# Kernel optimization log

Hardware: AMD Instinct MI355X
Metric: run time of the kernel (lower is better)

## Reference

```python
import jax, jax.numpy as jnp
import numpy as np

N_TOKEN = 392
POS_WEIGHT = 1.0
LOSS_WEIGHT = 1.0


def _cam_map(logits, w_proj, xf, shape):
    # logits: (B, K_cls); w_proj: (K_cls, C); xf: (B, C, N)
    B, T, H, W = shape
    top_cls = jnp.argmax(logits, axis=1)                 # sort desc -> [0] == argmax
    w_top = w_proj[top_cls]                              # (B, C) gather top-class weight row
    row = jnp.einsum('bc,bcn->bn', w_top, xf)            # (B, N) per-sample CAM scores
    mn = row.min(axis=1, keepdims=True)
    mx = row.max(axis=1, keepdims=True)
    rown = (row - mn) / (mx - mn)                        # min-max normalize
    vals, idxs = jax.lax.top_k(rown, N_TOKEN)            # (B, 392)
    hw = H * W
    ti = idxs // hw
    hi = (idxs % hw) // W
    wi = idxs % W
    bi = jnp.broadcast_to(jnp.arange(B)[:, None], idxs.shape)
    cam = jnp.zeros((B, T, H, W), rown.dtype).at[bi, ti, hi, wi].set(vals)
    return cam


def _forward(x, pred_v_logits, pred_n_logits, w_proj_v, w_proj_n,
             conv_w, conv_b, score_w, score_b):
    B, C, T, H, W = x.shape
    xf = x.reshape(B, C, T * H * W)
    cam_v = _cam_map(pred_v_logits, w_proj_v, xf, (B, T, H, W))
    cam_n = _cam_map(pred_n_logits, w_proj_n, xf, (B, T, H, W))
    cam_gt = jnp.maximum(cam_v, cam_n)                   # torch.where(v > n, v, n)
    cam_gt = jax.lax.stop_gradient(cam_gt)               # original builds it from numpy + .detach()

    dn = ('NCDHW', 'OIDHW', 'NCDHW')
    h1 = jax.nn.relu(
        jax.lax.conv_general_dilated(x, conv_w, (1, 1, 1),
                                     [(0, 0), (1, 1), (1, 1)],
                                     dimension_numbers=dn)
        + conv_b[None, :, None, None, None])
    logits = (jax.lax.conv_general_dilated(h1, score_w, (1, 1, 1),
                                           [(0, 0), (0, 0), (0, 0)],
                                           dimension_numbers=dn)
              + score_b[None, :, None, None, None])      # (B,1,T,H,W)

    xcam = logits[:, 0].reshape(B * T, H * W)
    y = cam_gt.reshape(B * T, H * W)
    # BCEWithLogitsLoss(pos_weight) mean
    bce = -(POS_WEIGHT * y * jax.nn.log_sigmoid(xcam)
            + (1.0 - y) * jax.nn.log_sigmoid(-xcam))
    return LOSS_WEIGHT * bce.mean()


def setup_inputs() -> dict:
    key = jax.random.key(0)
    ks = jax.random.split(key, 8)
    B, C, T, H, W = 64, 256, 32, 7, 7
    Kv, Kn, D = 97, 300, 512
    x = jax.random.normal(ks[0], (B, C, T, H, W), jnp.float32)
    pred_v_logits = jax.random.normal(ks[1], (B, Kv), jnp.float32)
    pred_n_logits = jax.random.normal(ks[2], (B, Kn), jnp.float32)
    w_proj_v = jax.random.normal(ks[3], (Kv, C), jnp.float32) / np.sqrt(C)
    w_proj_n = jax.random.normal(ks[4], (Kn, C), jnp.float32) / np.sqrt(C)
    conv_w = jax.random.normal(ks[5], (D, C, 1, 3, 3), jnp.float32) / np.sqrt(C * 9)
    conv_b = jnp.zeros((D,), jnp.float32)
    score_w = jax.random.normal(ks[6], (1, D, 1, 1, 1), jnp.float32) / np.sqrt(D)
    score_b = jnp.zeros((1,), jnp.float32)
    return {"x": x, "pred_v_logits": pred_v_logits, "pred_n_logits": pred_n_logits,
            "w_proj_v": w_proj_v, "w_proj_n": w_proj_n,
            "conv_w": conv_w, "conv_b": conv_b,
            "score_w": score_w, "score_b": score_b}


def reference(x, pred_v_logits, pred_n_logits, w_proj_v, w_proj_n,
              conv_w, conv_b, score_w, score_b):
    return _forward(x, pred_v_logits, pred_n_logits, w_proj_v, w_proj_n,
                    conv_w, conv_b, score_w, score_b)
```

## Files before the change

### kernel.cpp

```cpp
#include <hip/hip_runtime.h>
#include <hip/hip_bf16.h>
#include <math.h>

#define BB 64
#define CC 256
#define TT 32
#define HH 7
#define WW 7
#define HW 49
#define NN 1568
#define KV 97
#define KN 300
#define DD 512
#define NTOK 392
#define TOTAL (BB*TT*HW)
#define BCAP 256

typedef float f32x4 __attribute__((ext_vector_type(4)));
typedef short bf16x8 __attribute__((ext_vector_type(8)));

#define GLDS(g, l) __builtin_amdgcn_global_load_lds(                          \
    (const __attribute__((address_space(1))) void*)(g),                       \
    (__attribute__((address_space(3))) void*)(l), 16, 0, 0)

__global__ __launch_bounds__(256, 3) void k_tr(
        const float* __restrict__ x, __hip_bfloat16* __restrict__ xp,
        const float* __restrict__ cw, __hip_bfloat16* __restrict__ wb,
        int* __restrict__ counter) {
    __shared__ unsigned short xs[98 * 256];
    int bid = blockIdx.x;
    int tid = threadIdx.x;
    if (bid == 0 && tid == 0) *counter = 0;

    {
        int base = bid * 1152;
        #pragma unroll
        for (int r = 0; r < 5; ++r) {
            int o = base + r * 256 + tid;
            if (o < base + 1152) {
                int kk = o / (DD * CC);
                int rem = o - kk * (DD * CC);
                int d = rem >> 8, c = rem & 255;
                wb[o] = __float2bfloat16(cw[(d * CC + c) * 9 + kk]);
            }
        }
    }

    int b  = bid >> 4;
    int tp = bid & 15;
    int t0 = tp << 1;

    const float2* src = (const float2*)(x + ((size_t)(b * CC + tid) * TT + t0) * HW);
    #pragma unroll 1
    for (int r = 0; r < 6; ++r) {
        float2 v[8];
        #pragma unroll
        for (int j = 0; j < 8; ++j) v[j] = src[r * 8 + j];
        #pragma unroll
        for (int j = 0; j < 8; ++j) {
            int q = (r * 8 + j) * 2;
            __hip_bfloat16 b0 = __float2bfloat16(v[j].x);
            __hip_bfloat16 b1 = __float2bfloat16(v[j].y);
            xs[q * 256 + tid] = *reinterpret_cast<unsigned short*>(&b0);
            xs[(q + 1) * 256 + tid] = *reinterpret_cast<unsigned short*>(&b1);
        }
    }
    {
        float2 v = src[48];
        __hip_bfloat16 b0 = __float2bfloat16(v.x);
        __hip_bfloat16 b1 = __float2bfloat16(v.y);
        xs[96 * 256 + tid] = *reinterpret_cast<unsigned short*>(&b0);
        xs[97 * 256 + tid] = *reinterpret_cast<unsigned short*>(&b1);
    }
    __syncthreads();

    __hip_bfloat16* xpb = xp + (size_t)(b * TT + t0) * 81 * 256;
    const bf16x8 zero = (bf16x8){0, 0, 0, 0, 0, 0, 0, 0};
    for (int u = tid; u < 5184; u += 256) {
        int pos = u >> 5, c0 = (u & 31) * 8;
        int f = pos / 81, p = pos - f * 81;
        int hh = p / 9, ww = p - (p / 9) * 9;
        bf16x8 val = zero;
        if (hh >= 1 && hh <= 7 && ww >= 1 && ww <= 7) {
            int q = f * 49 + (hh - 1) * 7 + (ww - 1);
            val = *reinterpret_cast<const bf16x8*>(xs + q * 256 + c0);
        }
        *reinterpret_cast<bf16x8*>(xpb + (size_t)u * 8) = val;
    }
}

__device__ __forceinline__ int binof(float v) {
    int i = (int)(v * 1024.f);
    return i < 0 ? 0 : (i > 1023 ? 1023 : i);
}

__device__ void cam_block(int b, int tid, char* smem,
                          const float* __restrict__ x,
                          const float* __restrict__ pv, const float* __restrict__ pn,
                          const float* __restrict__ wpv, const float* __restrict__ wpn,
                          float* __restrict__ cam) {
    float* rv = (float*)smem;
    float* rn = (float*)(smem + 6272);
    int* h = (int*)(smem + 12544);
    int* tsum = (int*)(smem + 16640);
    float* lval_v = (float*)(smem + 17664);
    int* lidx_v = (int*)(smem + 18688);
    float* lval_n = (float*)(smem + 19712);
    int* lidx_n = (int*)(smem + 20736);
    float* wred = (float*)(smem + 21760);
    int* sc = (int*)(smem + 21824);
    float* wvs = (float*)(smem + 21888);
    float* wns = (float*)(smem + 22912);
    int* cls2 = (int*)(smem + 23936);

    int lane = tid & 63;
    if (tid < 128) {
        int head = tid >> 6;
        const float* r = head ? (pn + b * KN) : (pv + b * KV);
        int K = head ? KN : KV;
        float best = -1e30f; int bi = 0x7fffffff;
        for (int k = lane; k < K; k += 64) {
            float v = r[k];
            if (v > best || (v == best && k < bi)) { best = v; bi = k; }
        }
        #pragma unroll
        for (int off = 32; off >= 1; off >>= 1) {
            float ov = __shfl_xor(best, off);
            int oi = __shfl_xor(bi, off);
            if (ov > best || (ov == best && oi < bi)) { best = ov; bi = oi; }
        }
        if (lane == 0) cls2[head] = bi;
    }
    __syncthreads();
    wvs[tid] = wpv[cls2[0] * CC + tid];
    wns[tid] = wpn[cls2[1] * CC + tid];
    __syncthreads();

    {
        const f32x4* xb4 = (const f32x4*)(x + (size_t)b * CC * NN);
        bool two = tid < (392 - 256);
        f32x4 av0 = {0.f,0.f,0.f,0.f}, an0 = {0.f,0.f,0.f,0.f};
        f32x4 av1 = {0.f,0.f,0.f,0.f}, an1 = {0.f,0.f,0.f,0.f};
        for (int c = 0; c < CC; ++c) {
            float wv = wvs[c], wn = wns[c];
            const f32x4* rowc = xb4 + (size_t)c * 392;
            f32x4 u0 = rowc[tid];
            #pragma unroll
            for (int r = 0; r < 4; ++r) {
                av0[r] = fmaf(wv, u0[r], av0[r]);
                an0[r] = fmaf(wn, u0[r], an0[r]);
            }
            if (two) {
                f32x4 u1 = rowc[tid + 256];
                #pragma unroll
                for (int r = 0; r < 4; ++r) {
                    av1[r] = fmaf(wv, u1[r], av1[r]);
                    an1[r] = fmaf(wn, u1[r], an1[r]);
                }
            }
        }
        *reinterpret_cast<f32x4*>(rv + 4 * tid) = av0;
        *reinterpret_cast<f32x4*>(rn + 4 * tid) = an0;
        if (two) {
            *reinterpret_cast<f32x4*>(rv + 4 * (tid + 256)) = av1;
            *reinterpret_cast<f32x4*>(rn + 4 * (tid + 256)) = an1;
        }
    }
    __syncthreads();

    float mnv = 1e30f, mxv = -1e30f, mnn = 1e30f, mxn = -1e30f;
    for (int n = tid; n < NN; n += 256) {
        float v = rv[n]; mnv = fminf(mnv, v); mxv = fmaxf(mxv, v);
        float u = rn[n]; mnn = fminf(mnn, u); mxn = fmaxf(mxn, u);
    }
    #pragma unroll
    for (int off = 32; off >= 1; off >>= 1) {
        mnv = fminf(mnv, __shfl_xor(mnv, off));
        mxv = fmaxf(mxv, __shfl_xor(mxv, off));
        mnn = fminf(mnn, __shfl_xor(mnn, off));
        mxn = fmaxf(mxn, __shfl_xor(mxn, off));
    }
    if ((tid & 63) == 0) {
        int wid = tid >> 6;
        wred[wid * 4 + 0] = mnv; wred[wid * 4 + 1] = mxv;
        wred[wid * 4 + 2] = mnn; wred[wid * 4 + 3] = mxn;
    }
    if (tid == 0) { sc[0] = 0; sc[1] = 0; }
    __syncthreads();
    mnv = fminf(fminf(wred[0], wred[4]), fminf(wred[8], wred[12]));
    mxv = fmaxf(fmaxf(wred[1], wred[5]), fmaxf(wred[9], wred[13]));
    mnn = fminf(fminf(wred[2], wred[6]), fminf(wred[10], wred[14]));
    mxn = fmaxf(fmaxf(wred[3], wred[7]), fmaxf(wred[11], wred[15]));
    float iv = 1.f / (mxv - mnv), inn = 1.f / (mxn - mnn);

    for (int n = tid; n < NN; n += 256) {
        rv[n] = (rv[n] - mnv) * iv;
        rn[n] = (rn[n] - mnn) * inn;
    }
    for (int i = tid; i < 1024; i += 256) h[i] = 0;
    __syncthreads();
    for (int n = tid; n < NN; n += 256) {
        atomicAdd(&h[binof(rv[n])], 1);
        atomicAdd(&h[binof(rn[n])], 1 << 16);
    }
    __syncthreads();

    int h0 = h[4 * tid], h1 = h[4 * tid + 1], h2 = h[4 * tid + 2], h3 = h[4 * tid + 3];
    tsum[tid] = h0 + h1 + h2 + h3;
    __syncthreads();
    for (int off = 1; off < 256; off <<= 1) {
        int add = (tid + off < 256) ? tsum[tid + off] : 0;
        __syncthreads();
        tsum[tid] += add;
        __syncthreads();
    }
    {
        int scur = tsum[tid];
        int hk[4] = {h0, h1, h2, h3};
        #pragma unroll
        for (int k = 0; k < 4; ++k) {
            int snext = scur - hk[k];
            int scv = scur & 0xffff, ncv = snext & 0xffff;
            int sh = scur >> 16, nh = snext >> 16;
            if (scv >= NTOK && ncv < NTOK) { sc[2] = 4 * tid + k; sc[3] = ncv; }
            if (sh >= NTOK && nh < NTOK) { sc[4] = 4 * tid + k; sc[5] = nh; }
            scur = snext;
        }
    }
    __syncthreads();
    int bsv = sc[2], abv = sc[3], bsn = sc[4], abn = sc[5];

    for (int n = tid; n < NN; n += 256) {
        float v = rv[n]; int bv = binof(v);
        if (bv < bsv) rv[n] = 0.f;
        else if (bv == bsv) {
            int s = atomicAdd(&sc[0], 1);
            if (s < BCAP) { lval_v[s] = v; lidx_v[s] = n; }
        }
        float u = rn[n]; int bu = binof(u);
        if (bu < bsn) rn[n] = 0.f;
        else if (bu == bsn) {
            int s = atomicAdd(&sc[1], 1);
            if (s < BCAP) { lval_n[s] = u; lidx_n[s] = n; }
        }
    }
    __syncthreads();
    int Lv = sc[0] < BCAP ? sc[0] : BCAP;
    int Ln = sc[1] < BCAP ? sc[1] : BCAP;
    for (int i = tid; i < Lv; i += 256) {
        float vi = lval_v[i]; int ni = lidx_v[i]; int r = 0;
        for (int j = 0; j < Lv; ++j) {
            float vj = lval_v[j]; int nj = lidx_v[j];
            r += (vj > vi || (vj == vi && nj < ni)) ? 1 : 0;
        }
        rv[ni] = (r < NTOK - abv) ? vi : 0.f;
    }
    for (int i = tid; i < Ln; i += 256) {
        float vi = lval_n[i]; int ni = lidx_n[i]; int r = 0;
        for (int j = 0; j < Ln; ++j) {
            float vj = lval_n[j]; int nj = lidx_n[j];
            r += (vj > vi || (vj == vi && nj < ni)) ? 1 : 0;
        }
        rn[ni] = (r < NTOK - abn) ? vi : 0.f;
    }
    __syncthreads();
    for (int n = tid; n < NN; n += 256) cam[b * NN + n] = fmaxf(rv[n], rn[n]);
}

__global__ __launch_bounds__(256, 3) void k_gemm(
        const __hip_bfloat16* __restrict__ xp, const __hip_bfloat16* __restrict__ wb,
        const float* __restrict__ convb, const float* __restrict__ scorew,
        float* __restrict__ pl,
        const float* __restrict__ x,
        const float* __restrict__ pv, const float* __restrict__ pn,
        const float* __restrict__ wpv, const float* __restrict__ wpn,
        float* __restrict__ cam) {
    __shared__ char smem[32768];
    int tid = threadIdx.x;
    int bid = blockIdx.x;
    if (bid < 64) { cam_block(bid, tid, smem, x, pv, pn, wpv, wpn, cam); return; }
    char* As = smem;
    char* Bs = smem + 16384;
    int gid = bid - 64;
    int xcd = gid & 7;
    int local = gid >> 3;
    int mtile = xcd * 98 + (local >> 2);
    int nblk = local & 3;
    int m0 = mtile * 128;
    int n0 = nblk * 128;
    int lane = tid & 63, wv = tid >> 6;
    int wm = wv >> 1, wn = wv & 1;
    int ln = lane & 15, qd = lane >> 4;

    int rrow = tid >> 3;
    int segst = ((tid & 7) ^ (rrow & 7)) * 8;
    int bt_[4], hh_[4], ww_[4];
    const __hip_bfloat16* bptr[4];
    #pragma unroll
    for (int j = 0; j < 4; ++j) {
        int m = m0 + j * 32 + rrow;
        int bt = m / HW, q = m - bt * HW;
        bt_[j] = bt; hh_[j] = q / WW; ww_[j] = q - (q / WW) * WW;
        bptr[j] = wb + (size_t)(n0 + j * 32 + rrow) * 256 + segst;
    }

    int swz = ln & 7;
    int offk[2] = {((0 + qd) ^ swz) * 16, ((4 + qd) ^ swz) * 16};

    f32x4 acc[4][4];
    #pragma unroll
    for (int i = 0; i < 4; ++i)
        #pragma unroll
        for (int j = 0; j < 4; ++j) acc[i][j] = (f32x4){0.f, 0.f, 0.f, 0.f};

    for (int kk = 0; kk < 9; ++kk) {
        int kh = kk / 3, kw = kk - (kk / 3) * 3;
        const __hip_bfloat16* aptr[4];
        #pragma unroll
        for (int j = 0; j < 4; ++j)
            aptr[j] = xp + ((size_t)bt_[j] * 81 + (hh_[j] + kh) * 9 + (ww_[j] + kw)) * 256 + segst;
        const size_t boff = (size_t)kk * (DD * 256);
        #pragma unroll
        for (int c0 = 0; c0 < 256; c0 += 64) {
            __syncthreads();
            #pragma unroll
            for (int j = 0; j < 4; ++j) {
                GLDS(aptr[j] + c0, As + j * 4096 + tid * 16);
                GLDS(bptr[j] + boff + c0, Bs + j * 4096 + tid * 16);
            }
            __syncthreads();
            #pragma unroll
            for (int k2 = 0; k2 < 2; ++k2) {
                bf16x8 af[4], bfr[4];
                #pragma unroll
                for (int i = 0; i < 4; ++i)
                    af[i] = *(const bf16x8*)(As + (wm * 64 + i * 16 + ln) * 128 + offk[k2]);
                #pragma unroll
                for (int j = 0; j < 4; ++j)
                    bfr[j] = *(const bf16x8*)(Bs + (wn * 64 + j * 16 + ln) * 128 + offk[k2]);
                #pragma unroll
                for (int i = 0; i < 4; ++i)
                    #pragma unroll
                    for (int j = 0; j < 4; ++j)
                        acc[i][j] = __builtin_amdgcn_mfma_f32_16x16x32_bf16(af[i], bfr[j], acc[i][j], 0, 0, 0);
            }
        }
    }

    float swr[4], cbr[4];
    #pragma unroll
    for (int j = 0; j < 4; ++j) {
        int n = n0 + wn * 64 + j * 16 + ln;
        swr[j] = scorew[n];
        cbr[j] = convb[n];
    }
    float* dst = pl + (size_t)(nblk * 2 + wn) * TOTAL;
    #pragma unroll
    for (int i = 0; i < 4; ++i) {
        #pragma unroll
        for (int r = 0; r < 4; ++r) {
            float v = 0.f;
            #pragma unroll
            for (int j = 0; j < 4; ++j) {
                float h1 = acc[i][j][r] + cbr[j];
                h1 = h1 > 0.f ? h1 : 0.f;
                v = fmaf(swr[j], h1, v);
            }
            v += __shfl_xor(v, 1);
            v += __shfl_xor(v, 2);
            v += __shfl_xor(v, 4);
            v += __shfl_xor(v, 8);
            if (ln == 0)
                dst[m0 + wm * 64 + i * 16 + qd * 4 + r] = v;
        }
    }
}

__global__ __launch_bounds__(256) void k_bce(
        const float* __restrict__ pl, const float* __restrict__ cam,
        const float* __restrict__ sb, float* __restrict__ part,
        int* __restrict__ counter, float* __restrict__ out) {
    __shared__ float sbuf[256];
    __shared__ int isLast;
    int tid = threadIdx.x;
    int m = blockIdx.x * 256 + tid;
    float l = sb[0];
    #pragma unroll
    for (int s = 0; s < 8; ++s) l += pl[(size_t)s * TOTAL + m];
    float y = cam[m];
    float v = fmaxf(l, 0.f) - l * y + log1pf(expf(-fabsf(l)));
    sbuf[tid] = v; __syncthreads();
    for (int k = 128; k > 0; k >>= 1) {
        if (tid < k) sbuf[tid] += sbuf[tid + k];
        __syncthreads();
    }
    if (tid == 0) {
        part[blockIdx.x] = sbuf[0];
        __threadfence();
        int d = atomicAdd(counter, 1);
        isLast = (d == 391);
    }
    __syncthreads();
    if (isLast) {
        float s = 0.f;
        for (int i = tid; i < 392; i += 256) s += part[i];
        sbuf[tid] = s; __syncthreads();
        for (int k = 128; k > 0; k >>= 1) {
            if (tid < k) sbuf[tid] += sbuf[tid + k];
            __syncthreads();
        }
        if (tid == 0) out[0] = sbuf[0] * (1.0f / (float)TOTAL);
    }
}

extern "C" void kernel_launch(void* const* d_in, const int* in_sizes, int n_in,
                              void* d_out, int out_size, void* d_ws, size_t ws_size,
                              hipStream_t stream) {
    const float* x   = (const float*)d_in[0];
    const float* pv  = (const float*)d_in[1];
    const float* pn  = (const float*)d_in[2];
    const float* wpv = (const float*)d_in[3];
    const float* wpn = (const float*)d_in[4];
    const float* cw  = (const float*)d_in[5];
    const float* cb  = (const float*)d_in[6];
    const float* sw  = (const float*)d_in[7];
    const float* sb  = (const float*)d_in[8];

    char* w8 = (char*)d_ws;
    __hip_bfloat16* xp  = (__hip_bfloat16*)w8;
    __hip_bfloat16* wb  = (__hip_bfloat16*)(w8 + 84934656);
    float* pl      = (float*)(w8 + 87293952);
    float* cam     = (float*)(w8 + 90505216);
    float* part    = (float*)(w8 + 90906624);
    int*   counter = (int*)(w8 + 90908192);

    k_tr<<<1024, 256, 0, stream>>>(x, xp, cw, wb, counter);
    k_gemm<<<64 + 3136, 256, 0, stream>>>(xp, wb, cb, sw, pl,
                                          x, pv, pn, wpv, wpn, cam);
    k_bce<<<392, 256, 0, stream>>>(pl, cam, sb, part, counter, (float*)d_out);
}
```

Before: 432.7 us.

## Move CAM into transpose kernel and rebuild conv GEMM as 8-wave triple-buffered pipeline

The CAM blocks move out of the GEMM launch and into the transpose/pad kernel, so the GEMM grid is uniform. The conv GEMM becomes a 512-thread, 256x128-tile kernel with a three-slot LDS ring filled by direct global-to-LDS loads issued two stages ahead. Each stage is split into four MFMA phases that interleave fragment reads and next-stage loads, using barriers, waitcnt, sched_barrier and setprio to overlap memory with compute. The costs are much larger shared memory per block (lower occupancy), more barriers, and the epilogue must now handle the new tile mapping correctly.

```diff
diff --git a/kernel.cpp b/kernel.cpp
--- a/kernel.cpp
+++ b/kernel.cpp
@@ -23,71 +23,7 @@
     (const __attribute__((address_space(1))) void*)(g),                       \
     (__attribute__((address_space(3))) void*)(l), 16, 0, 0)
 
-__global__ __launch_bounds__(256, 3) void k_tr(
-        const float* __restrict__ x, __hip_bfloat16* __restrict__ xp,
-        const float* __restrict__ cw, __hip_bfloat16* __restrict__ wb,
-        int* __restrict__ counter) {
-    __shared__ unsigned short xs[98 * 256];
-    int bid = blockIdx.x;
-    int tid = threadIdx.x;
-    if (bid == 0 && tid == 0) *counter = 0;
-
-    {
-        int base = bid * 1152;
-        #pragma unroll
-        for (int r = 0; r < 5; ++r) {
-            int o = base + r * 256 + tid;
-            if (o < base + 1152) {
-                int kk = o / (DD * CC);
-                int rem = o - kk * (DD * CC);
-                int d = rem >> 8, c = rem & 255;
-                wb[o] = __float2bfloat16(cw[(d * CC + c) * 9 + kk]);
-            }
-        }
-    }
-
-    int b  = bid >> 4;
-    int tp = bid & 15;
-    int t0 = tp << 1;
-
-    const float2* src = (const float2*)(x + ((size_t)(b * CC + tid) * TT + t0) * HW);
-    #pragma unroll 1
-    for (int r = 0; r < 6; ++r) {
-        float2 v[8];
-        #pragma unroll
-        for (int j = 0; j < 8; ++j) v[j] = src[r * 8 + j];
-        #pragma unroll
-        for (int j = 0; j < 8; ++j) {
-            int q = (r * 8 + j) * 2;
-            __hip_bfloat16 b0 = __float2bfloat16(v[j].x);
-            __hip_bfloat16 b1 = __float2bfloat16(v[j].y);
-            xs[q * 256 + tid] = *reinterpret_cast<unsigned short*>(&b0);
-            xs[(q + 1) * 256 + tid] = *reinterpret_cast<unsigned short*>(&b1);
-        }
-    }
-    {
-        float2 v = src[48];
-        __hip_bfloat16 b0 = __float2bfloat16(v.x);
-        __hip_bfloat16 b1 = __float2bfloat16(v.y);
-        xs[96 * 256 + tid] = *reinterpret_cast<unsigned short*>(&b0);
-        xs[97 * 256 + tid] = *reinterpret_cast<unsigned short*>(&b1);
-    }
-    __syncthreads();
-
-    __hip_bfloat16* xpb = xp + (size_t)(b * TT + t0) * 81 * 256;
-    const bf16x8 zero = (bf16x8){0, 0, 0, 0, 0, 0, 0, 0};
-    for (int u = tid; u < 5184; u += 256) {
-        int pos = u >> 5, c0 = (u & 31) * 8;
-        int f = pos / 81, p = pos - f * 81;
-        int hh = p / 9, ww = p - (p / 9) * 9;
-        bf16x8 val = zero;
-        if (hh >= 1 && hh <= 7 && ww >= 1 && ww <= 7) {
-            int q = f * 49 + (hh - 1) * 7 + (ww - 1);
-            val = *reinterpret_cast<const bf16x8*>(xs + q * 256 + c0);
-        }
-        *reinterpret_cast<bf16x8*>(xpb + (size_t)u * 8) = val;
-    }
-}
+#define MFMA16(a, b, c) __builtin_amdgcn_mfma_f32_16x16x32_bf16(a, b, c, 0, 0, 0)
 
 __device__ __forceinline__ int binof(float v) {
     int i = (int)(v * 1024.f);
@@ -267,84 +203,227 @@
     for (int n = tid; n < NN; n += 256) cam[b * NN + n] = fmaxf(rv[n], rn[n]);
 }
 
-__global__ __launch_bounds__(256, 3) void k_gemm(
+__global__ __launch_bounds__(256, 3) void k_trcam(
+        const float* __restrict__ x, __hip_bfloat16* __restrict__ xp,
+        const float* __restrict__ cw, __hip_bfloat16* __restrict__ wb,
+        const float* __restrict__ pv, const float* __restrict__ pn,
+        const float* __restrict__ wpv, const float* __restrict__ wpn,
+        float* __restrict__ cam, int* __restrict__ counter) {
+    __shared__ char smem[50176];
+    int bid0 = blockIdx.x;
+    int tid = threadIdx.x;
+    if (bid0 < 64) { cam_block(bid0, tid, smem, x, pv, pn, wpv, wpn, cam); return; }
+    int bid = bid0 - 64;
+    unsigned short* xs = (unsigned short*)smem;
+    if (bid == 0 && tid == 0) *counter = 0;
+
+    {
+        int base = bid * 1152;
+        #pragma unroll
+        for (int r = 0; r < 5; ++r) {
+            int o = base + r * 256 + tid;
+            if (o < base + 1152) {
+                int kk = o / (DD * CC);
+                int rem = o - kk * (DD * CC);
+                int d = rem >> 8, c = rem & 255;
+                wb[o] = __float2bfloat16(cw[(d * CC + c) * 9 + kk]);
+            }
+        }
+    }
+
+    int b  = bid >> 4;
+    int tp = bid & 15;
+    int t0 = tp << 1;
+
+    const float2* src = (const float2*)(x + ((size_t)(b * CC + tid) * TT + t0) * HW);
+    #pragma unroll 1
+    for (int r = 0; r < 6; ++r) {
+        float2 v[8];
+        #pragma unroll
+        for (int j = 0; j < 8; ++j) v[j] = src[r * 8 + j];
+        #pragma unroll
+        for (int j = 0; j < 8; ++j) {
+            int q = (r * 8 + j) * 2;
+            __hip_bfloat16 b0 = __float2bfloat16(v[j].x);
+            __hip_bfloat16 b1 = __float2bfloat16(v[j].y);
+            xs[q * 256 + tid] = *reinterpret_cast<unsigned short*>(&b0);
+            xs[(q + 1) * 256 + tid] = *reinterpret_cast<unsigned short*>(&b1);
+        }
+    }
+    {
+        float2 v = src[48];
+        __hip_bfloat16 b0 = __float2bfloat16(v.x);
+        __hip_bfloat16 b1 = __float2bfloat16(v.y);
+        xs[96 * 256 + tid] = *reinterpret_cast<unsigned short*>(&b0);
+        xs[97 * 256 + tid] = *reinterpret_cast<unsigned short*>(&b1);
+    }
+    __syncthreads();
+
+    __hip_bfloat16* xpb = xp + (size_t)(b * TT + t0) * 81 * 256;
+    const bf16x8 zero = (bf16x8){0, 0, 0, 0, 0, 0, 0, 0};
+    for (int u = tid; u < 5184; u += 256) {
+        int pos = u >> 5, c0 = (u & 31) * 8;
+        int f = pos / 81, p = pos - f * 81;
+        int hh = p / 9, ww = p - (p / 9) * 9;
+        bf16x8 val = zero;
+        if (hh >= 1 && hh <= 7 && ww >= 1 && ww <= 7) {
+            int q = f * 49 + (hh - 1) * 7 + (ww - 1);
+            val = *reinterpret_cast<const bf16x8*>(xs + q * 256 + c0);
+        }
+        *reinterpret_cast<bf16x8*>(xpb + (size_t)u * 8) = val;
+    }
+}
+
+__global__ __launch_bounds__(512, 2) void k_gemm8(
         const __hip_bfloat16* __restrict__ xp, const __hip_bfloat16* __restrict__ wb,
         const float* __restrict__ convb, const float* __restrict__ scorew,
-        float* __restrict__ pl,
-        const float* __restrict__ x,
-        const float* __restrict__ pv, const float* __restrict__ pn,
-        const float* __restrict__ wpv, const float* __restrict__ wpn,
-        float* __restrict__ cam) {
-    __shared__ char smem[32768];
+        float* __restrict__ pl) {
+    __shared__ char smem[147456];
     int tid = threadIdx.x;
     int bid = blockIdx.x;
-    if (bid < 64) { cam_block(bid, tid, smem, x, pv, pn, wpv, wpn, cam); return; }
-    char* As = smem;
-    char* Bs = smem + 16384;
-    int gid = bid - 64;
-    int xcd = gid & 7;
-    int local = gid >> 3;
-    int mtile = xcd * 98 + (local >> 2);
+    int xcd = bid & 7;
+    int local = bid >> 3;
+    int mtile = xcd * 49 + (local >> 2);
     int nblk = local & 3;
-    int m0 = mtile * 128;
+    int m0 = mtile * 256;
     int n0 = nblk * 128;
     int lane = tid & 63, wv = tid >> 6;
     int wm = wv >> 1, wn = wv & 1;
     int ln = lane & 15, qd = lane >> 4;
-
-    int rrow = tid >> 3;
-    int segst = ((tid & 7) ^ (rrow & 7)) * 8;
-    int bt_[4], hh_[4], ww_[4];
-    const __hip_bfloat16* bptr[4];
-    #pragma unroll
-    for (int j = 0; j < 4; ++j) {
-        int m = m0 + j * 32 + rrow;
-        int bt = m / HW, q = m - bt * HW;
-        bt_[j] = bt; hh_[j] = q / WW; ww_[j] = q - (q / WW) * WW;
-        bptr[j] = wb + (size_t)(n0 + j * 32 + rrow) * 256 + segst;
-    }
-
     int swz = ln & 7;
+
+    int srow = tid >> 3, sseg = tid & 7;
+    int swseg = (sseg ^ (srow & 7)) * 8;
+    unsigned aoff[4];
+    #pragma unroll
+    for (int q = 0; q < 4; ++q) {
+        int m = m0 + q * 64 + srow;
+        int bt = m / HW, qq = m - bt * HW;
+        int hh = qq / WW, ww = qq - (qq / WW) * WW;
+        aoff[q] = (unsigned)(bt * 81 + (hh + 1) * 9 + (ww + 1) - 10) * 256 + swseg;
+    }
+    unsigned boff[2];
+    #pragma unroll
+    for (int q = 0; q < 2; ++q)
+        boff[q] = (unsigned)(n0 + q * 64 + srow) * 256 + swseg;
+
+    auto STAGE = [&](int s, int part) {
+        int kk = s >> 2;
+        int kh = kk / 3, kw = kk - kh * 3;
+        unsigned c0 = (unsigned)((s & 3) << 6);
+        int buf = s - (s / 3) * 3;
+        char* base = smem + buf * 49152;
+        if (part < 2) {
+            unsigned so = (unsigned)(kh * 9 + kw) * 256 + c0;
+            #pragma unroll
+            for (int u = 0; u < 2; ++u) {
+                int q = part * 2 + u;
+                GLDS(xp + (size_t)(aoff[q] + so), base + q * 8192 + tid * 16);
+            }
+        } else {
+            unsigned so = (unsigned)kk * (DD * 256) + c0;
+            #pragma unroll
+            for (int u = 0; u < 2; ++u)
+                GLDS(wb + (size_t)(boff[u] + so), base + 32768 + u * 8192 + tid * 16);
+        }
+    };
+
+    f32x4 acc[4][4];
+    #pragma unroll
+    for (int i = 0; i < 4; ++i)
+        #pragma unroll
+        for (int j = 0; j < 4; ++j) acc[i][j] = (f32x4){0.f, 0.f, 0.f, 0.f};
+
     int offk[2] = {((0 + qd) ^ swz) * 16, ((4 + qd) ^ swz) * 16};
 
-    f32x4 acc[4][4];
-    #pragma unroll
-    for (int i = 0; i < 4; ++i)
-        #pragma unroll
-        for (int j = 0; j < 4; ++j) acc[i][j] = (f32x4){0.f, 0.f, 0.f, 0.f};
-
-    for (int kk = 0; kk < 9; ++kk) {
-        int kh = kk / 3, kw = kk - (kk / 3) * 3;
-        const __hip_bfloat16* aptr[4];
-        #pragma unroll
-        for (int j = 0; j < 4; ++j)
-            aptr[j] = xp + ((size_t)bt_[j] * 81 + (hh_[j] + kh) * 9 + (ww_[j] + kw)) * 256 + segst;
-        const size_t boff = (size_t)kk * (DD * 256);
-        #pragma unroll
-        for (int c0 = 0; c0 < 256; c0 += 64) {
-            __syncthreads();
-            #pragma unroll
-            for (int j = 0; j < 4; ++j) {
-                GLDS(aptr[j] + c0, As + j * 4096 + tid * 16);
-                GLDS(bptr[j] + boff + c0, Bs + j * 4096 + tid * 16);
-            }
-            __syncthreads();
-            #pragma unroll
-            for (int k2 = 0; k2 < 2; ++k2) {
-                bf16x8 af[4], bfr[4];
+    STAGE(0, 0); STAGE(0, 1); STAGE(0, 2);
+    STAGE(1, 0); STAGE(1, 1); STAGE(1, 2);
+    asm volatile("s_waitcnt vmcnt(6)" ::: "memory");
+    __builtin_amdgcn_s_barrier();
+
+    #pragma unroll 1
+    for (int s = 0; s < 36; ++s) {
+        const char* Ab = smem + (s - (s / 3) * 3) * 49152;
+        const char* Bb = Ab + 32768;
+        bool more = s < 34;
+        bf16x8 af[2][2], b0r[2][2], b1r[2][2];
+
+        #pragma unroll
+        for (int i = 0; i < 2; ++i)
+            #pragma unroll
+            for (int k2 = 0; k2 < 2; ++k2)
+                af[i][k2] = *(const bf16x8*)(Ab + (wm * 64 + i * 16 + ln) * 128 + offk[k2]);
+        #pragma unroll
+        for (int j = 0; j < 2; ++j)
+            #pragma unroll
+            for (int k2 = 0; k2 < 2; ++k2)
+                b0r[j][k2] = *(const bf16x8*)(Bb + (wn * 64 + j * 16 + ln) * 128 + offk[k2]);
+        if (more) STAGE(s + 2, 0);
+        __builtin_amdgcn_s_barrier();
+        asm volatile("s_waitcnt lgkmcnt(0)" ::: "memory");
+        __builtin_amdgcn_sched_barrier(0);
+        __builtin_amdgcn_s_setprio(1);
+        #pragma unroll
+        for (int i = 0; i < 2; ++i)
+            #pragma unroll
+            for (int j = 0; j < 2; ++j)
                 #pragma unroll
-                for (int i = 0; i < 4; ++i)
-                    af[i] = *(const bf16x8*)(As + (wm * 64 + i * 16 + ln) * 128 + offk[k2]);
+                for (int k2 = 0; k2 < 2; ++k2)
+                    acc[i][j] = MFMA16(af[i][k2], b0r[j][k2], acc[i][j]);
+        __builtin_amdgcn_s_setprio(0);
+
+        #pragma unroll
+        for (int j = 0; j < 2; ++j)
+            #pragma unroll
+            for (int k2 = 0; k2 < 2; ++k2)
+                b1r[j][k2] = *(const bf16x8*)(Bb + (wn * 64 + (j + 2) * 16 + ln) * 128 + offk[k2]);
+        if (more) STAGE(s + 2, 1);
+        __builtin_amdgcn_s_barrier();
+        asm volatile("s_waitcnt lgkmcnt(0)" ::: "memory");
+        __builtin_amdgcn_sched_barrier(0);
+        __builtin_amdgcn_s_setprio(1);
+        #pragma unroll
+        for (int i = 0; i < 2; ++i)
+            #pragma unroll
+            for (int j = 0; j < 2; ++j)
                 #pragma unroll
-                for (int j = 0; j < 4; ++j)
-                    bfr[j] = *(const bf16x8*)(Bs + (wn * 64 + j * 16 + ln) * 128 + offk[k2]);
+                for (int k2 = 0; k2 < 2; ++k2)
+                    acc[i][j + 2] = MFMA16(af[i][k2], b1r[j][k2], acc[i][j + 2]);
+        __builtin_amdgcn_s_setprio(0);
+
+        #pragma unroll
+        for (int i = 0; i < 2; ++i)
+            #pragma unroll
+            for (int k2 = 0; k2 < 2; ++k2)
+                af[i][k2] = *(const bf16x8*)(Ab + (wm * 64 + (i + 2) * 16 + ln) * 128 + offk[k2]);
+        if (more) STAGE(s + 2, 2);
+        __builtin_amdgcn_s_barrier();
+        asm volatile("s_waitcnt lgkmcnt(0)" ::: "memory");
+        __builtin_amdgcn_sched_barrier(0);
+        __builtin_amdgcn_s_setprio(1);
+        #pragma unroll
+        for (int i = 0; i < 2; ++i)
+            #pragma unroll
+            for (int j = 0; j < 2; ++j)
                 #pragma unroll
-                for (int i = 0; i < 4; ++i)
-                    #pragma unroll
-                    for (int j = 0; j < 4; ++j)
-                        acc[i][j] = __builtin_amdgcn_mfma_f32_16x16x32_bf16(af[i], bfr[j], acc[i][j], 0, 0, 0);
-            }
-        }
+                for (int k2 = 0; k2 < 2; ++k2)
+                    acc[i + 2][j] = MFMA16(af[i][k2], b0r[j][k2], acc[i + 2][j]);
+        __builtin_amdgcn_s_setprio(0);
+
+        __builtin_amdgcn_s_barrier();
+        __builtin_amdgcn_s_setprio(1);
+        #pragma unroll
+        for (int i = 0; i < 2; ++i)
+            #pragma unroll
+            for (int j = 0; j < 2; ++j)
+                #pragma unroll
+                for (int k2 = 0; k2 < 2; ++k2)
+                    acc[i + 2][j + 2] = MFMA16(af[i][k2], b1r[j][k2], acc[i + 2][j + 2]);
+        __builtin_amdgcn_s_setprio(0);
+
+        if (more) asm volatile("s_waitcnt vmcnt(6)" ::: "memory");
+        else      asm volatile("s_waitcnt vmcnt(0)" ::: "memory");
+        __builtin_amdgcn_s_barrier();
     }
 
     float swr[4], cbr[4];
@@ -434,8 +513,8 @@
     float* part    = (float*)(w8 + 90906624);
     int*   counter = (int*)(w8 + 90908192);
 
-    k_tr<<<1024, 256, 0, stream>>>(x, xp, cw, wb, counter);
-    k_gemm<<<64 + 3136, 256, 0, stream>>>(xp, wb, cb, sw, pl,
-                                          x, pv, pn, wpv, wpn, cam);
+    k_trcam<<<64 + 1024, 256, 0, stream>>>(x, xp, cw, wb, pv, pn, wpv, wpn,
+                                           cam, counter);
+    k_gemm8<<<1568, 512, 0, stream>>>(xp, wb, cb, sw, pl);
     k_bce<<<392, 256, 0, stream>>>(pl, cam, sb, part, counter, (float*)d_out);
 }
```

Result: slower. 554.5 us (+28.1%).
